# Performance work log

Measured on AMD Instinct MI355X. Metric: run time of the kernel, lower is better.

## Reference

```python
import math
import jax, jax.numpy as jnp
import numpy as np

B, C, K, P, STRIDE, ITERS = 32, 32, 3, 4, 2, 3
PSIZE = P * P
EPS = 1e-6
LAMBDA = 1e-3
LN_2PI = math.log(2.0 * math.pi)


def _extract_patches(x, K, stride):
    # Replicates torch F.unfold + transpose + view exactly, including the
    # layout reinterpretation: unfold's channel dim is ordered (c, kh, kw)
    # (c slowest) but the torch code views it as (K*K, c).
    b, h, w, c = x.shape
    pad = K // 2
    oh = (h + 2 * pad - K) // stride + 1
    ow = (w + 2 * pad - K) // stride + 1
    xp = jnp.pad(x, ((0, 0), (pad, pad), (pad, pad), (0, 0)))
    sl = []
    for kh in range(K):
        for kw in range(K):
            sl.append(xp[:, kh:kh + stride * (oh - 1) + 1:stride,
                            kw:kw + stride * (ow - 1) + 1:stride, :])
    p = jnp.stack(sl, axis=-1)                 # (b, oh, ow, c, K*K)  -> (c, kh, kw) order
    p = p.reshape(b, oh, ow, c * K * K)        # flat, c slowest (matches torch unfold memory)
    patches = p.reshape(b, oh, ow, K * K, c)   # reinterpret as (K*K, c), as the torch view does
    return patches, oh, ow


def _em_routing(v, a_in, beta_u, beta_a):
    # v: (b, Bin, C, psize), a_in: (b, Bin, 1)
    b, Bin, Cc, psize = v.shape
    r = jnp.full((b, Bin, Cc, 1), 1.0 / Cc, dtype=v.dtype)
    a4 = a_in[:, :, None, :]                   # (b, Bin, 1, 1)
    a_out = None
    mu = None
    for t in range(ITERS):
        # ---- M step ----
        rr = r * a4
        rr = rr / (jnp.sum(rr, axis=2, keepdims=True) + EPS)
        r_sum = jnp.sum(rr, axis=1, keepdims=True)            # (b,1,C,1)
        coeff = rr / (r_sum + EPS)
        mu = jnp.sum(coeff * v, axis=1, keepdims=True)        # (b,1,C,psize)
        sigma_sq = jnp.sum(coeff * (v - mu) ** 2, axis=1, keepdims=True) + EPS
        sigma_sq = jnp.maximum(sigma_sq, 1e-4)
        r_sum_flat = r_sum.reshape(b, Cc, 1)
        sig_flat = jnp.maximum(sigma_sq.reshape(b, Cc, psize), 1e-4)
        cost_h = (beta_u.reshape(1, Cc, 1) + jnp.log(jnp.sqrt(sig_flat))) * r_sum_flat
        a_out = jax.nn.sigmoid(LAMBDA * (beta_a.reshape(1, Cc) - jnp.sum(cost_h, axis=2)))
        a_out = jnp.clip(a_out, 1e-4, 1.0 - 1e-4)
        mu = jnp.nan_to_num(mu, nan=0.0, posinf=1e4, neginf=-1e4)
        sigma_sq = jnp.nan_to_num(sigma_sq, nan=1e-4, posinf=1e4, neginf=1e-4)
        a_out = jnp.nan_to_num(a_out, nan=0.5, posinf=1.0 - 1e-4, neginf=1e-4)
        # ---- E step ----
        if t < ITERS - 1:
            ss = jnp.maximum(sigma_sq, 1e-4)
            ao = jnp.clip(a_out, 1e-4, 1.0 - 1e-4)
            ln_p = -(v - mu) ** 2 / (2.0 * ss) - jnp.log(jnp.sqrt(ss)) - 0.5 * LN_2PI
            ln_ap = jnp.sum(ln_p, axis=3) + jnp.log(ao.reshape(b, 1, Cc) + EPS)
            ln_ap = jnp.nan_to_num(ln_ap, nan=0.0, posinf=50.0, neginf=-50.0)
            r = jax.nn.softmax(ln_ap, axis=2)[..., None]
            r = jnp.nan_to_num(r, nan=1.0 / Cc, posinf=1.0, neginf=0.0)
    p_out = jnp.nan_to_num(mu[:, 0], nan=0.0, posinf=1e4, neginf=-1e4)  # (b, C, psize)
    a_out = jnp.nan_to_num(a_out, nan=0.5, posinf=1.0 - 1e-4, neginf=1e-4)
    return p_out, a_out


def setup_inputs() -> dict:
    key = jax.random.key(0)
    k1, k2 = jax.random.split(key)
    x = jax.random.normal(k1, (2, 16, 16, B * (PSIZE + 1)), dtype=jnp.float32)
    weights = jax.random.normal(k2, (1, K * K * B, C, PSIZE, PSIZE), dtype=jnp.float32) * 0.02
    beta_u = jnp.zeros((C,), dtype=jnp.float32)
    beta_a = jnp.zeros((C,), dtype=jnp.float32)
    return {"x": x, "weights": weights, "beta_u": beta_u, "beta_a": beta_a}


def reference(x, weights, beta_u, beta_a):
    b, h, w, c = x.shape
    patches, oh, ow = _extract_patches(x, K, STRIDE)          # (b,oh,ow,K*K,c)
    p_in = patches[..., :B * PSIZE].reshape(b * oh * ow, K * K * B, PSIZE)
    a_in = patches[..., B * PSIZE:].reshape(b * oh * ow, K * K * B, 1)
    w0 = weights[0]                                           # (K*K*B, C, psize, psize)
    v = jnp.einsum('bip,icpq->bicq', p_in, w0)                # (b*, K*K*B, C, psize)
    p_out, a_out = _em_routing(v, a_in, beta_u, beta_a)
    p_out = p_out.reshape(b, oh, ow, C * PSIZE)
    a_out = a_out.reshape(b, oh, ow, C)
    out = jnp.concatenate([p_out, a_out], axis=3)
    return p_out, a_out, out
```

## Files before the change

### kernel.cpp

```cpp
#include <hip/hip_runtime.h>
#include <hip/hip_bf16.h>
#include <math.h>

#define EPSV 1e-6f
#define LAMBDAV 1e-3f
#define LN_2PI 1.8378770664093453f

__device__ __forceinline__ float bflo(unsigned int u) {
    union { unsigned int i; float f; } x; x.i = u << 16; return x.f;
}
__device__ __forceinline__ float bfhi(unsigned int u) {
    union { unsigned int i; float f; } x; x.i = u & 0xffff0000u; return x.f;
}
__device__ __forceinline__ unsigned short f2bf(float f) {
    __hip_bfloat16 h = __float2bfloat16(f);
    return *(unsigned short*)&h;
}

typedef __attribute__((ext_vector_type(8))) short s8v;
typedef __attribute__((ext_vector_type(4))) float f4v;
typedef __attribute__((ext_vector_type(2))) int i2v;

template<int CTRL>
__device__ __forceinline__ float dpp_mv(float x) {
    return __int_as_float(__builtin_amdgcn_update_dpp(
        0, __float_as_int(x), CTRL, 0xF, 0xF, true));
}
__device__ __forceinline__ float x16_sum(float x) {
#if __has_builtin(__builtin_amdgcn_permlane16_swap)
    i2v r = __builtin_amdgcn_permlane16_swap(__float_as_int(x), __float_as_int(x), false, false);
    return __int_as_float(r.x) + __int_as_float(r.y);
#else
    return x + __int_as_float(__builtin_amdgcn_ds_swizzle(__float_as_int(x), 0x401F));
#endif
}
__device__ __forceinline__ float x16_max(float x) {
#if __has_builtin(__builtin_amdgcn_permlane16_swap)
    i2v r = __builtin_amdgcn_permlane16_swap(__float_as_int(x), __float_as_int(x), false, false);
    return fmaxf(__int_as_float(r.x), __int_as_float(r.y));
#else
    return fmaxf(x, __int_as_float(__builtin_amdgcn_ds_swizzle(__float_as_int(x), 0x401F)));
#endif
}
__device__ __forceinline__ float xhalf_sum(float x) {
#if __has_builtin(__builtin_amdgcn_permlane32_swap)
    i2v r = __builtin_amdgcn_permlane32_swap(__float_as_int(x), __float_as_int(x), false, false);
    return __int_as_float(r.x) + __int_as_float(r.y);
#else
    return x + __shfl_xor(x, 32, 64);
#endif
}
__device__ __forceinline__ float red_max32(float x) {
    x = fmaxf(x, dpp_mv<0xB1>(x));
    x = fmaxf(x, dpp_mv<0x4E>(x));
    x = fmaxf(x, dpp_mv<0x124>(x));
    x = fmaxf(x, dpp_mv<0x128>(x));
    return x16_max(x);
}
__device__ __forceinline__ float red_sum32(float x) {
    x += dpp_mv<0xB1>(x);
    x += dpp_mv<0x4E>(x);
    x += dpp_mv<0x124>(x);
    x += dpp_mv<0x128>(x);
    return x16_sum(x);
}
__device__ __forceinline__ float red_sum16(float x) {
    x += dpp_mv<0xB1>(x);
    x += dpp_mv<0x4E>(x);
    x += dpp_mv<0x124>(x);
    x += dpp_mv<0x128>(x);
    return x;
}

__global__ __launch_bounds__(256)
void conv_v_kernel(const float* __restrict__ x, const float* __restrict__ w,
                   __hip_bfloat16* __restrict__ vout)
{
    __shared__ unsigned short wb[256 * 40];
    __shared__ unsigned short pb[128 * 40];

    const int bid = blockIdx.x;
    const int i2  = bid >> 1;
    const int mh  = bid & 1;
    const int tid = threadIdx.x;

    for (int u = tid; u < 256 * 8; u += 256) {
        int r = u >> 3, j = u & 7;
        *(unsigned int*)&wb[r * 40 + 16 + j * 2] = 0;
    }
    for (int u = tid; u < 128 * 8; u += 256) {
        int r = u >> 3, j = u & 7;
        *(unsigned int*)&pb[r * 40 + 16 + j * 2] = 0;
    }
    #pragma unroll 4
    for (int u = 0; u < 16; ++u) {
        int idx = u * 256 + tid;
        int cl = idx >> 8, p = (idx >> 4) & 15, q = idx & 15;
        wb[(cl * 16 + q) * 40 + p] = f2bf(w[(size_t)i2 * 8192 + mh * 4096 + idx]);
    }
    #pragma unroll
    for (int u = 0; u < 8; ++u) {
        int idx = u * 256 + tid;
        int nn = idx >> 4, p = idx & 15;
        int e  = i2 * 16 + p;
        int k2 = e >> 9, c2 = e & 511;
        int f  = k2 * 544 + c2;
        int ci = f / 9, kk = f - ci * 9;
        int bi = nn >> 6, oi = (nn >> 3) & 7, oj = nn & 7;
        int row = 2 * oi + kk / 3 - 1;
        int col = 2 * oj + (kk - (kk / 3) * 3) - 1;
        float val = 0.f;
        if ((unsigned)row < 16u && (unsigned)col < 16u)
            val = x[((bi * 16 + row) * 16 + col) * 544 + ci];
        pb[nn * 40 + p] = f2bf(val);
    }
    __syncthreads();

    const int lane = tid & 63;
    const int wv   = tid >> 6;
    const int l16  = lane & 15;
    const int quad = lane >> 4;
    const int cq0l = wv * 64;

    s8v afrag[4], bfrag[8];
    #pragma unroll
    for (int mt = 0; mt < 4; ++mt)
        afrag[mt] = *(const s8v*)&wb[(cq0l + mt * 16 + l16) * 40 + quad * 8];
    #pragma unroll
    for (int nt = 0; nt < 8; ++nt)
        bfrag[nt] = *(const s8v*)&pb[(nt * 16 + l16) * 40 + quad * 8];

    #pragma unroll
    for (int nt = 0; nt < 8; ++nt) {
        const int nl = nt * 16 + l16;
        #pragma unroll
        for (int mt = 0; mt < 4; ++mt) {
            f4v acc = {0.f, 0.f, 0.f, 0.f};
            acc = __builtin_amdgcn_mfma_f32_16x16x32_bf16(afrag[mt], bfrag[nt], acc, 0, 0, 0);
            int cq = mh * 256 + cq0l + mt * 16 + quad * 4;
            unsigned int lo = f2bf(acc[0]) | ((unsigned int)f2bf(acc[1]) << 16);
            unsigned int hi = f2bf(acc[2]) | ((unsigned int)f2bf(acc[3]) << 16);
            uint2 pk; pk.x = lo; pk.y = hi;
            *(uint2*)((unsigned short*)vout + ((size_t)nl * 288 + i2) * 512 + cq) = pk;
        }
    }
}

__global__ __launch_bounds__(1024, 4)
void em_routing_kernel(const float* __restrict__ x,
                       const unsigned short* __restrict__ v,
                       const float* __restrict__ beta_u,
                       const float* __restrict__ beta_a,
                       float* __restrict__ out)
{
    __shared__ float fct_s[288];
    __shared__ float red_s[16 * 64 * 17];
    __shared__ float mu_s[32 * 17];
    __shared__ float i2ss_s[32 * 17];
    __shared__ float aout_s[32];
    __shared__ float kc_s[32];

    const int n   = blockIdx.x;
    const int tid = threadIdx.x;
    const int bi = n >> 6, oi = (n >> 3) & 7, oj = n & 7;

    if (tid < 288) {
        int k2 = tid >> 5;
        int c2 = 512 + (tid & 31);
        int f  = k2 * 544 + c2;
        int ci = f / 9;
        int kk = f - ci * 9;
        int row = 2 * oi + kk / 3 - 1;
        int col = 2 * oj + (kk - (kk / 3) * 3) - 1;
        float a = 0.f;
        if ((unsigned)row < 16u && (unsigned)col < 16u)
            a = x[((bi * 16 + row) * 16 + col) * 544 + ci];
        fct_s[tid] = a / (a + EPSV);
    }
    __syncthreads();

    const unsigned short* vb = v + (size_t)n * 288 * 512;
    const int wv   = tid >> 6;
    const int lane = tid & 63;
    const int c    = lane & 31;
    const int qh   = lane >> 5;
    const int qb   = qh * 8;
    const unsigned short* base = vb + c * 16 + qb;

    for (int t = 0; t < 3; ++t) {
        float mu8[8], is8[8], kcv = 0.f;
        if (t > 0) {
            #pragma unroll
            for (int j = 0; j < 8; ++j) {
                mu8[j] = mu_s[c * 17 + qb + j];
                is8[j] = i2ss_s[c * 17 + qb + j];
            }
            kcv = kc_s[c];
        }

        float s0 = 0.f, s1[8], s2[8];
        #pragma unroll
        for (int j = 0; j < 8; ++j) { s1[j] = 0.f; s2[j] = 0.f; }

        uint4 ua = *(const uint4*)(base + (size_t)(0 * 16 + wv) * 512);
        uint4 ub = *(const uint4*)(base + (size_t)(1 * 16 + wv) * 512);

        for (int kp = 0; kp < 9; ++kp) {
            const int ia = (2 * kp) * 16 + wv;
            const int ib = (2 * kp + 1) * 16 + wv;
            uint4 una, unb;
            if (kp < 8) {
                una = *(const uint4*)(base + (size_t)((2 * kp + 2) * 16 + wv) * 512);
                unb = *(const uint4*)(base + (size_t)((2 * kp + 3) * 16 + wv) * 512);
            }
            float va[8], vvb[8];
            va[0] = bflo(ua.x); va[1] = bfhi(ua.x);
            va[2] = bflo(ua.y); va[3] = bfhi(ua.y);
            va[4] = bflo(ua.z); va[5] = bfhi(ua.z);
            va[6] = bflo(ua.w); va[7] = bfhi(ua.w);
            vvb[0] = bflo(ub.x); vvb[1] = bfhi(ub.x);
            vvb[2] = bflo(ub.y); vvb[3] = bfhi(ub.y);
            vvb[4] = bflo(ub.z); vvb[5] = bfhi(ub.z);
            vvb[6] = bflo(ub.w); vvb[7] = bfhi(ub.w);

            float rra, rrb;
            if (t == 0) {
                rra = fct_s[ia] * 0.03125f;
                rrb = fct_s[ib] * 0.03125f;
            } else {
                float pa = 0.f, pb2 = 0.f;
                #pragma unroll
                for (int j = 0; j < 8; ++j) {
                    float da = va[j] - mu8[j];
                    float db = vvb[j] - mu8[j];
                    pa  += da * da * is8[j];
                    pb2 += db * db * is8[j];
                }
                pa  = xhalf_sum(pa);
                pb2 = xhalf_sum(pb2);
                float acca = kcv - pa;
                float accb = kcv - pb2;
                float mxa = red_max32(acca);
                float mxb = red_max32(accb);
                float ea = __expf(acca - mxa);
                float eb = __expf(accb - mxb);
                float sa = red_sum32(ea);
                float sb = red_sum32(eb);
                rra = (ea / sa) * fct_s[ia];
                rrb = (eb / sb) * fct_s[ib];
            }

            s0 += rra + rrb;
            #pragma unroll
            for (int j = 0; j < 8; ++j) {
                s1[j] += rra * va[j] + rrb * vvb[j];
                s2[j] += rra * va[j] * va[j] + rrb * vvb[j] * vvb[j];
            }
            ua = una; ub = unb;
        }

        {
            float* dst = &red_s[(wv * 64 + lane) * 17];
            dst[0] = s0;
            #pragma unroll
            for (int j = 0; j < 8; ++j) { dst[1 + j] = s1[j]; dst[9 + j] = s2[j]; }
        }
        __syncthreads();

        if (tid < 512) {
            const int c2 = tid >> 4, q2 = tid & 15;
            const int qh2 = q2 >> 3, j2 = q2 & 7;
            float S0 = 0.f, S1 = 0.f, S2 = 0.f;
            #pragma unroll
            for (int wvi = 0; wvi < 16; ++wvi) {
                S0 += red_s[(wvi * 64 + c2) * 17];
                const float* sp = &red_s[(wvi * 64 + qh2 * 32 + c2) * 17];
                S1 += sp[1 + j2];
                S2 += sp[9 + j2];
            }
            float invr = 1.0f / (S0 + EPSV);
            float w0  = S0 * invr;
            float m   = S1 * invr;
            float s2p = S2 * invr;
            float sig = s2p - m * m * (2.0f - w0);
            sig = fmaxf(sig + EPSV, 1e-4f);
            float hl = 0.5f * logf(sig);
            mu_s[c2 * 17 + q2]   = m;
            i2ss_s[c2 * 17 + q2] = 1.0f / (2.0f * sig);
            float shl = red_sum16(hl);
            if (q2 == 0) {
                float bu  = beta_u[c2];
                float cs  = (16.0f * bu + shl) * S0;
                float arg = LAMBDAV * (beta_a[c2] - cs);
                float ao  = 1.0f / (1.0f + expf(-arg));
                ao = fminf(fmaxf(ao, 1e-4f), 1.0f - 1e-4f);
                aout_s[c2] = ao;
                kc_s[c2]   = logf(ao + EPSV) - shl - 8.0f * LN_2PI;
            }
        }
        __syncthreads();
    }

    if (tid < 512) {
        int c2 = tid >> 4, q2 = tid & 15;
        float mu = mu_s[c2 * 17 + q2];
        if (isnan(mu)) mu = 0.f;
        mu = fminf(fmaxf(mu, -10000.f), 10000.f);
        out[(size_t)n * 512 + tid] = mu;
        out[69632 + (size_t)n * 544 + tid] = mu;
        if (tid < 32) {
            float ao = aout_s[tid];
            if (isnan(ao)) ao = 0.5f;
            out[65536 + n * 32 + tid] = ao;
            out[69632 + n * 544 + 512 + tid] = ao;
        }
    }
}

extern "C" void kernel_launch(void* const* d_in, const int* in_sizes, int n_in,
                              void* d_out, int out_size, void* d_ws, size_t ws_size,
                              hipStream_t stream) {
    const float* x  = (const float*)d_in[0];
    const float* w  = (const float*)d_in[1];
    const float* bu = (const float*)d_in[2];
    const float* ba = (const float*)d_in[3];
    float* out = (float*)d_out;
    __hip_bfloat16* v = (__hip_bfloat16*)d_ws;

    conv_v_kernel<<<dim3(576), dim3(256), 0, stream>>>(x, w, v);
    em_routing_kernel<<<dim3(128), dim3(1024), 0, stream>>>(
        x, (const unsigned short*)v, bu, ba, out);
}
```

Baseline: 122.3 us.

## Split EM routing across two blocks per position with per-iteration launches

Splits each position's input-capsule reduction across two blocks, so 256 blocks run per EM iteration instead of 128. The iterations become separate kernel launches that exchange partial sums through a global workspace, and a small final kernel computes the outputs. This aims to use more compute units, at the cost of extra launch overhead and global-memory traffic for the partials.

```diff
diff --git a/kernel.cpp b/kernel.cpp
--- a/kernel.cpp
+++ b/kernel.cpp
@@ -147,20 +147,22 @@
 }
 
 __global__ __launch_bounds__(1024, 4)
-void em_routing_kernel(const float* __restrict__ x,
-                       const unsigned short* __restrict__ v,
-                       const float* __restrict__ beta_u,
-                       const float* __restrict__ beta_a,
-                       float* __restrict__ out)
+void em_sweep_kernel(const float* __restrict__ x,
+                     const unsigned short* __restrict__ v,
+                     const float* __restrict__ beta_u,
+                     const float* __restrict__ beta_a,
+                     float* __restrict__ gpart,
+                     const int t)
 {
     __shared__ float fct_s[288];
     __shared__ float red_s[16 * 64 * 17];
     __shared__ float mu_s[32 * 17];
     __shared__ float i2ss_s[32 * 17];
-    __shared__ float aout_s[32];
     __shared__ float kc_s[32];
 
-    const int n   = blockIdx.x;
+    const int bid = blockIdx.x;
+    const int n   = bid & 127;
+    const int h   = bid >> 7;
     const int tid = threadIdx.x;
     const int bi = n >> 6, oi = (n >> 3) & 7, oj = n & 7;
 
@@ -177,6 +179,32 @@
             a = x[((bi * 16 + row) * 16 + col) * 544 + ci];
         fct_s[tid] = a / (a + EPSV);
     }
+
+    if (t > 0 && tid < 512) {
+        const int c2 = tid >> 4, q2 = tid & 15;
+        const float* pa = gpart + ((size_t)(t - 1) * 128 + n) * 2 * 1088;
+        float S1 = pa[tid] + pa[1088 + tid];
+        float S2 = pa[512 + tid] + pa[1088 + 512 + tid];
+        float S0 = pa[1024 + c2] + pa[1088 + 1024 + c2];
+        float invr = 1.0f / (S0 + EPSV);
+        float w0  = S0 * invr;
+        float m   = S1 * invr;
+        float s2p = S2 * invr;
+        float sig = s2p - m * m * (2.0f - w0);
+        sig = fmaxf(sig + EPSV, 1e-4f);
+        float hl = 0.5f * logf(sig);
+        mu_s[c2 * 17 + q2]   = m;
+        i2ss_s[c2 * 17 + q2] = 1.0f / (2.0f * sig);
+        float shl = red_sum16(hl);
+        if (q2 == 0) {
+            float bu  = beta_u[c2];
+            float cs  = (16.0f * bu + shl) * S0;
+            float arg = LAMBDAV * (beta_a[c2] - cs);
+            float ao  = 1.0f / (1.0f + expf(-arg));
+            ao = fminf(fmaxf(ao, 1e-4f), 1.0f - 1e-4f);
+            kc_s[c2]  = logf(ao + EPSV) - shl - 8.0f * LN_2PI;
+        }
+    }
     __syncthreads();
 
     const unsigned short* vb = v + (size_t)n * 288 * 512;
@@ -187,133 +215,148 @@
     const int qb   = qh * 8;
     const unsigned short* base = vb + c * 16 + qb;
 
-    for (int t = 0; t < 3; ++t) {
-        float mu8[8], is8[8], kcv = 0.f;
-        if (t > 0) {
+    float mu8[8], is8[8], kcv = 0.f;
+    if (t > 0) {
+        #pragma unroll
+        for (int j = 0; j < 8; ++j) {
+            mu8[j] = mu_s[c * 17 + qb + j];
+            is8[j] = i2ss_s[c * 17 + qb + j];
+        }
+        kcv = kc_s[c];
+    }
+
+    float s0 = 0.f, s1[8], s2[8];
+    #pragma unroll
+    for (int j = 0; j < 8; ++j) { s1[j] = 0.f; s2[j] = 0.f; }
+
+    const int kofs  = h * 10;
+    const int npair = 5 - h;
+
+    uint4 ua = *(const uint4*)(base + (size_t)((kofs + 0) * 16 + wv) * 512);
+    uint4 ub = *(const uint4*)(base + (size_t)((kofs + 1) * 16 + wv) * 512);
+
+    for (int kp = 0; kp < npair; ++kp) {
+        const int ia = (kofs + 2 * kp) * 16 + wv;
+        const int ib = ia + 16;
+        uint4 una = ua, unb = ub;
+        if (kp + 1 < npair) {
+            una = *(const uint4*)(base + (size_t)(ia + 32) * 512);
+            unb = *(const uint4*)(base + (size_t)(ia + 48) * 512);
+        }
+        float va[8], vvb[8];
+        va[0] = bflo(ua.x); va[1] = bfhi(ua.x);
+        va[2] = bflo(ua.y); va[3] = bfhi(ua.y);
+        va[4] = bflo(ua.z); va[5] = bfhi(ua.z);
+        va[6] = bflo(ua.w); va[7] = bfhi(ua.w);
+        vvb[0] = bflo(ub.x); vvb[1] = bfhi(ub.x);
+        vvb[2] = bflo(ub.y); vvb[3] = bfhi(ub.y);
+        vvb[4] = bflo(ub.z); vvb[5] = bfhi(ub.z);
+        vvb[6] = bflo(ub.w); vvb[7] = bfhi(ub.w);
+
+        float rra, rrb;
+        if (t == 0) {
+            rra = fct_s[ia] * 0.03125f;
+            rrb = fct_s[ib] * 0.03125f;
+        } else {
+            float pa = 0.f, pb2 = 0.f;
             #pragma unroll
             for (int j = 0; j < 8; ++j) {
-                mu8[j] = mu_s[c * 17 + qb + j];
-                is8[j] = i2ss_s[c * 17 + qb + j];
+                float da = va[j] - mu8[j];
+                float db = vvb[j] - mu8[j];
+                pa  += da * da * is8[j];
+                pb2 += db * db * is8[j];
             }
-            kcv = kc_s[c];
-        }
-
-        float s0 = 0.f, s1[8], s2[8];
-        #pragma unroll
-        for (int j = 0; j < 8; ++j) { s1[j] = 0.f; s2[j] = 0.f; }
-
-        uint4 ua = *(const uint4*)(base + (size_t)(0 * 16 + wv) * 512);
-        uint4 ub = *(const uint4*)(base + (size_t)(1 * 16 + wv) * 512);
-
-        for (int kp = 0; kp < 9; ++kp) {
-            const int ia = (2 * kp) * 16 + wv;
-            const int ib = (2 * kp + 1) * 16 + wv;
-            uint4 una, unb;
-            if (kp < 8) {
-                una = *(const uint4*)(base + (size_t)((2 * kp + 2) * 16 + wv) * 512);
-                unb = *(const uint4*)(base + (size_t)((2 * kp + 3) * 16 + wv) * 512);
-            }
-            float va[8], vvb[8];
-            va[0] = bflo(ua.x); va[1] = bfhi(ua.x);
-            va[2] = bflo(ua.y); va[3] = bfhi(ua.y);
-            va[4] = bflo(ua.z); va[5] = bfhi(ua.z);
-            va[6] = bflo(ua.w); va[7] = bfhi(ua.w);
-            vvb[0] = bflo(ub.x); vvb[1] = bfhi(ub.x);
-            vvb[2] = bflo(ub.y); vvb[3] = bfhi(ub.y);
-            vvb[4] = bflo(ub.z); vvb[5] = bfhi(ub.z);
-            vvb[6] = bflo(ub.w); vvb[7] = bfhi(ub.w);
-
-            float rra, rrb;
-            if (t == 0) {
-                rra = fct_s[ia] * 0.03125f;
-                rrb = fct_s[ib] * 0.03125f;
-            } else {
-                float pa = 0.f, pb2 = 0.f;
-                #pragma unroll
-                for (int j = 0; j < 8; ++j) {
-                    float da = va[j] - mu8[j];
-                    float db = vvb[j] - mu8[j];
-                    pa  += da * da * is8[j];
-                    pb2 += db * db * is8[j];
-                }
-                pa  = xhalf_sum(pa);
-                pb2 = xhalf_sum(pb2);
-                float acca = kcv - pa;
-                float accb = kcv - pb2;
-                float mxa = red_max32(acca);
-                float mxb = red_max32(accb);
-                float ea = __expf(acca - mxa);
-                float eb = __expf(accb - mxb);
-                float sa = red_sum32(ea);
-                float sb = red_sum32(eb);
-                rra = (ea / sa) * fct_s[ia];
-                rrb = (eb / sb) * fct_s[ib];
-            }
-
-            s0 += rra + rrb;
-            #pragma unroll
-            for (int j = 0; j < 8; ++j) {
-                s1[j] += rra * va[j] + rrb * vvb[j];
-                s2[j] += rra * va[j] * va[j] + rrb * vvb[j] * vvb[j];
-            }
-            ua = una; ub = unb;
-        }
-
-        {
-            float* dst = &red_s[(wv * 64 + lane) * 17];
-            dst[0] = s0;
-            #pragma unroll
-            for (int j = 0; j < 8; ++j) { dst[1 + j] = s1[j]; dst[9 + j] = s2[j]; }
-        }
-        __syncthreads();
-
-        if (tid < 512) {
-            const int c2 = tid >> 4, q2 = tid & 15;
-            const int qh2 = q2 >> 3, j2 = q2 & 7;
-            float S0 = 0.f, S1 = 0.f, S2 = 0.f;
-            #pragma unroll
-            for (int wvi = 0; wvi < 16; ++wvi) {
-                S0 += red_s[(wvi * 64 + c2) * 17];
-                const float* sp = &red_s[(wvi * 64 + qh2 * 32 + c2) * 17];
-                S1 += sp[1 + j2];
-                S2 += sp[9 + j2];
-            }
-            float invr = 1.0f / (S0 + EPSV);
-            float w0  = S0 * invr;
-            float m   = S1 * invr;
-            float s2p = S2 * invr;
-            float sig = s2p - m * m * (2.0f - w0);
-            sig = fmaxf(sig + EPSV, 1e-4f);
-            float hl = 0.5f * logf(sig);
-            mu_s[c2 * 17 + q2]   = m;
-            i2ss_s[c2 * 17 + q2] = 1.0f / (2.0f * sig);
-            float shl = red_sum16(hl);
-            if (q2 == 0) {
-                float bu  = beta_u[c2];
-                float cs  = (16.0f * bu + shl) * S0;
-                float arg = LAMBDAV * (beta_a[c2] - cs);
-                float ao  = 1.0f / (1.0f + expf(-arg));
-                ao = fminf(fmaxf(ao, 1e-4f), 1.0f - 1e-4f);
-                aout_s[c2] = ao;
-                kc_s[c2]   = logf(ao + EPSV) - shl - 8.0f * LN_2PI;
-            }
-        }
-        __syncthreads();
-    }
+            pa  = xhalf_sum(pa);
+            pb2 = xhalf_sum(pb2);
+            float acca = kcv - pa;
+            float accb = kcv - pb2;
+            float mxa = red_max32(acca);
+            float mxb = red_max32(accb);
+            float ea = __expf(acca - mxa);
+            float eb = __expf(accb - mxb);
+            float sa = red_sum32(ea);
+            float sb = red_sum32(eb);
+            rra = (ea / sa) * fct_s[ia];
+            rrb = (eb / sb) * fct_s[ib];
+        }
+
+        s0 += rra + rrb;
+        #pragma unroll
+        for (int j = 0; j < 8; ++j) {
+            s1[j] += rra * va[j] + rrb * vvb[j];
+            s2[j] += rra * va[j] * va[j] + rrb * vvb[j] * vvb[j];
+        }
+        ua = una; ub = unb;
+    }
+
+    {
+        float* dst = &red_s[(wv * 64 + lane) * 17];
+        dst[0] = s0;
+        #pragma unroll
+        for (int j = 0; j < 8; ++j) { dst[1 + j] = s1[j]; dst[9 + j] = s2[j]; }
+    }
+    __syncthreads();
 
     if (tid < 512) {
-        int c2 = tid >> 4, q2 = tid & 15;
-        float mu = mu_s[c2 * 17 + q2];
-        if (isnan(mu)) mu = 0.f;
-        mu = fminf(fmaxf(mu, -10000.f), 10000.f);
-        out[(size_t)n * 512 + tid] = mu;
-        out[69632 + (size_t)n * 544 + tid] = mu;
-        if (tid < 32) {
-            float ao = aout_s[tid];
-            if (isnan(ao)) ao = 0.5f;
-            out[65536 + n * 32 + tid] = ao;
-            out[69632 + n * 544 + 512 + tid] = ao;
-        }
+        const int c2 = tid >> 4, q2 = tid & 15;
+        const int qh2 = q2 >> 3, j2 = q2 & 7;
+        float S0 = 0.f, S1 = 0.f, S2 = 0.f;
+        #pragma unroll
+        for (int wvi = 0; wvi < 16; ++wvi) {
+            S0 += red_s[(wvi * 64 + c2) * 17];
+            const float* sp = &red_s[(wvi * 64 + qh2 * 32 + c2) * 17];
+            S1 += sp[1 + j2];
+            S2 += sp[9 + j2];
+        }
+        float* po = gpart + (((size_t)t * 128 + n) * 2 + h) * 1088;
+        po[tid] = S1;
+        po[512 + tid] = S2;
+        if (q2 == 0) po[1024 + c2] = S0;
+    }
+}
+
+__global__ __launch_bounds__(512)
+void em_final_kernel(const float* __restrict__ gpart,
+                     const float* __restrict__ beta_u,
+                     const float* __restrict__ beta_a,
+                     float* __restrict__ out)
+{
+    __shared__ float aout_s[32];
+    const int n   = blockIdx.x;
+    const int tid = threadIdx.x;
+    const int c2 = tid >> 4, q2 = tid & 15;
+
+    const float* pa = gpart + ((size_t)2 * 128 + n) * 2 * 1088;
+    float S1 = pa[tid] + pa[1088 + tid];
+    float S2 = pa[512 + tid] + pa[1088 + 512 + tid];
+    float S0 = pa[1024 + c2] + pa[1088 + 1024 + c2];
+    float invr = 1.0f / (S0 + EPSV);
+    float w0  = S0 * invr;
+    float m   = S1 * invr;
+    float s2p = S2 * invr;
+    float sig = s2p - m * m * (2.0f - w0);
+    sig = fmaxf(sig + EPSV, 1e-4f);
+    float hl = 0.5f * logf(sig);
+    float shl = red_sum16(hl);
+    if (q2 == 0) {
+        float bu  = beta_u[c2];
+        float cs  = (16.0f * bu + shl) * S0;
+        float arg = LAMBDAV * (beta_a[c2] - cs);
+        float ao  = 1.0f / (1.0f + expf(-arg));
+        ao = fminf(fmaxf(ao, 1e-4f), 1.0f - 1e-4f);
+        if (isnan(ao)) ao = 0.5f;
+        aout_s[c2] = ao;
+    }
+    float mu = m;
+    if (isnan(mu)) mu = 0.f;
+    mu = fminf(fmaxf(mu, -10000.f), 10000.f);
+    out[(size_t)n * 512 + tid] = mu;
+    out[69632 + (size_t)n * 544 + tid] = mu;
+    __syncthreads();
+    if (tid < 32) {
+        float ao = aout_s[tid];
+        out[65536 + n * 32 + tid] = ao;
+        out[69632 + n * 544 + 512 + tid] = ao;
     }
 }
 
@@ -326,8 +369,14 @@
     const float* ba = (const float*)d_in[3];
     float* out = (float*)d_out;
     __hip_bfloat16* v = (__hip_bfloat16*)d_ws;
+    float* gpart = (float*)((char*)d_ws + (40u << 20));
 
     conv_v_kernel<<<dim3(576), dim3(256), 0, stream>>>(x, w, v);
-    em_routing_kernel<<<dim3(128), dim3(1024), 0, stream>>>(
-        x, (const unsigned short*)v, bu, ba, out);
-}
+    em_sweep_kernel<<<dim3(256), dim3(1024), 0, stream>>>(
+        x, (const unsigned short*)v, bu, ba, gpart, 0);
+    em_sweep_kernel<<<dim3(256), dim3(1024), 0, stream>>>(
+        x, (const unsigned short*)v, bu, ba, gpart, 1);
+    em_sweep_kernel<<<dim3(256), dim3(1024), 0, stream>>>(
+        x, (const unsigned short*)v, bu, ba, gpart, 2);
+    em_final_kernel<<<dim3(128), dim3(512), 0, stream>>>(gpart, bu, ba, out);
+}
```

Measured after the change: 117.5 us. 3.9% less time.
